# Kernel tuning notes

Measured on AMD Instinct MI355X. Metric: run time of the kernel, lower is better.

The kernel has to match this reference:

```python
import jax, jax.numpy as jnp
import numpy as np

N_HEAD = 8
DROP_RATE = 0.1


def setup_inputs() -> dict:
    key = jax.random.key(0)
    k1, k2, k3 = jax.random.split(key, 3)
    n, c, h, w = 16, 512, 32, 32
    return {
        "x": jax.random.normal(k1, (n, c, h, w), jnp.float32),
        "qkv_w": jax.random.normal(k2, (3 * c, c), jnp.float32) * 0.02,
        "qkv_b": jnp.zeros((3 * c,), jnp.float32),
        "out_w": jax.random.normal(k3, (c, c), jnp.float32) * 0.02,
        "out_b": jnp.zeros((c,), jnp.float32),
        "dropout_enabled": 0,
    }


def reference(x, qkv_w, qkv_b, out_w, out_b, dropout_enabled):
    n, c, h, w = x.shape
    hd = c // N_HEAD  # head dim
    # fused QKV 1x1 conv == per-pixel matmul: [n, 3c, h, w]
    qkv = jnp.einsum('oc,nchw->nohw', qkv_w, x) + qkv_b[None, :, None, None]
    # [n, 3*n_head, hd, h*w] -> [n, 3*n_head, h*w, hd]
    qkv = jnp.swapaxes(qkv.reshape(n, N_HEAD * 3, hd, h * w), 2, 3)
    q, k, v = jnp.split(qkv, 3, axis=1)  # each [n, n_head, hw, hd]
    scale = hd ** (-0.25)
    att = jax.nn.softmax((q * scale) @ (jnp.swapaxes(k, 2, 3) * scale), axis=3)
    y = jnp.swapaxes(att @ v, 2, 3).reshape(n, c, h, w)
    y = jnp.einsum('oc,nchw->nohw', out_w, y) + out_b[None, :, None, None]
    # Dropout2d: drops whole (n, c) channel maps
    rate = DROP_RATE * dropout_enabled
    keep = jax.random.bernoulli(jax.random.key(42), 1.0 - rate, shape=(n, c))
    y = y * keep[..., None, None] / (1.0 - rate)
    return x + y
```

## Files before the change

kernel.cpp:

```cpp
#include <hip/hip_runtime.h>

typedef short bf16x8 __attribute__((ext_vector_type(8)));
typedef float f32x4 __attribute__((ext_vector_type(4)));
typedef float f32x16 __attribute__((ext_vector_type(16)));

#define MFMA16(a,b,c) __builtin_amdgcn_mfma_f32_16x16x32_bf16((a),(b),(c),0,0,0)
#define MFMA32(a,b,c) __builtin_amdgcn_mfma_f32_32x32x16_bf16((a),(b),(c),0,0,0)

static __device__ __forceinline__ unsigned short f2bf(float f){
  unsigned u; __builtin_memcpy(&u, &f, 4);
  u += 0x7fffu + ((u >> 16) & 1u);
  return (unsigned short)(u >> 16);
}

static __device__ __forceinline__ unsigned cvtpk(float lo, float hi){
  unsigned r;
  asm volatile("v_cvt_pk_bf16_f32 %0, %1, %2" : "=v"(r) : "v"(lo), "v"(hi));
  return r;
}
static __device__ __forceinline__ void pl32swap(unsigned &a, unsigned &b){
  asm volatile("v_permlane32_swap_b32 %0, %1" : "+v"(a), "+v"(b));
}

static __device__ __forceinline__ void gload_lds16(const void* g, void* l) {
  __builtin_amdgcn_global_load_lds(
      (__attribute__((address_space(1))) void*)g,
      (__attribute__((address_space(3))) void*)l, 16, 0, 0);
}

__global__ __launch_bounds__(256) void cvt_bf16(
    const float* __restrict__ in, unsigned short* __restrict__ out, int n) {
  int i = blockIdx.x * 256 + threadIdx.x;
  if (i < n) out[i] = f2bf(in[i]);
}

__global__ __launch_bounds__(256) void transpose_cvt(
    const float* __restrict__ in, unsigned short* __restrict__ out)
{
  __shared__ unsigned short tile[32][33];
  const long base = (long)blockIdx.z * 512 * 1024;
  const int t = threadIdx.x, tx = t & 31, ty = t >> 5;
  const int c0 = blockIdx.x * 32, r0 = blockIdx.y * 32;
  const float* ib = in + base;
#pragma unroll
  for (int i = 0; i < 4; ++i)
    tile[ty + i * 8][tx] = f2bf(ib[(long)(r0 + ty + i * 8) * 1024 + c0 + tx]);
  __syncthreads();
  unsigned short* ob = out + base;
#pragma unroll
  for (int i = 0; i < 4; ++i)
    ob[(long)(c0 + ty + i * 8) * 512 + r0 + tx] = tile[tx][ty + i * 8];
}

__global__ __launch_bounds__(256, 3) void gemm_qkv(
    const unsigned short* __restrict__ A, const unsigned short* __restrict__ B,
    unsigned short* __restrict__ qkvout, const float* __restrict__ bias)
{
  const int M = 1024, K = 512;
  __shared__ unsigned short As[128 * 64];
  __shared__ unsigned short Bs[128 * 64];
  const int t = threadIdx.x, lane = t & 63, wv = t >> 6;
  const int quad = lane >> 4, ln = lane & 15;
  const int m0 = blockIdx.y * 128, n0 = blockIdx.x * 128;
  const long zb = blockIdx.z;
  A += zb * (long)M * K;

  const int srow = wv * 32 + (lane >> 3);
  const int scol = ((lane & 7) * 8) ^ ((lane >> 3) * 8);

  f32x4 zero = {0.f, 0.f, 0.f, 0.f};
  f32x4 acc[4][4];
#pragma unroll
  for (int i = 0; i < 4; ++i)
#pragma unroll
    for (int j = 0; j < 4; ++j) acc[i][j] = zero;

  const int wm = (wv & 1) * 64, wn = (wv >> 1) * 64;
  const int rsw = (ln & 7) * 8;

  for (int kt = 0; kt < K; kt += 64) {
#pragma unroll
    for (int i = 0; i < 4; ++i) {
      gload_lds16(&A[(long)(m0 + srow + i * 8) * K + kt + scol],
                  &As[(wv * 32 + i * 8) * 64]);
      gload_lds16(&B[(long)(n0 + srow + i * 8) * K + kt + scol],
                  &Bs[(wv * 32 + i * 8) * 64]);
    }
    __syncthreads();
#pragma unroll
    for (int kk = 0; kk < 64; kk += 32) {
      bf16x8 a[4], b[4];
#pragma unroll
      for (int i = 0; i < 4; ++i)
        a[i] = *(const bf16x8*)&As[(wm + i * 16 + ln) * 64 + ((kk + quad * 8) ^ rsw)];
#pragma unroll
      for (int j = 0; j < 4; ++j)
        b[j] = *(const bf16x8*)&Bs[(wn + j * 16 + ln) * 64 + ((kk + quad * 8) ^ rsw)];
#pragma unroll
      for (int i = 0; i < 4; ++i)
#pragma unroll
        for (int j = 0; j < 4; ++j)
          acc[i][j] = MFMA16(a[i], b[j], acc[i][j]);
    }
    __syncthreads();
  }

#pragma unroll
  for (int j = 0; j < 4; ++j) {
    int o = n0 + wn + j * 16 + ln;
    float bb = bias[o];
    int part = o >> 9;
    int h = (o >> 6) & 7, d = o & 63;
    float qs = (part == 0) ? 0.18033688f : 1.0f;
#pragma unroll
    for (int i = 0; i < 4; ++i) {
      int p = m0 + wm + i * 16 + quad * 4;
      f32x4 v = acc[i][j];
      if (part < 2) {
        unsigned short* dst = qkvout + (long)part * 8388608
            + ((long)(zb * 8 + h) * 1024 + p) * 64 + d;
#pragma unroll
        for (int r = 0; r < 4; ++r) dst[r * 64] = f2bf((v[r] + bb) * qs);
      } else {
        long cidx = ((long)zb * 512 + (o - 1024)) * 1024 + p;
        ushort4 st;
        st.x = f2bf(v[0] + bb); st.y = f2bf(v[1] + bb);
        st.z = f2bf(v[2] + bb); st.w = f2bf(v[3] + bb);
        *(ushort4*)&qkvout[16777216 + cidx] = st;
      }
    }
  }
}

__global__ __launch_bounds__(256, 3) void gemm_out(
    const unsigned short* __restrict__ A, const unsigned short* __restrict__ B,
    float* __restrict__ C, const float* __restrict__ bias,
    const float* __restrict__ xin, const int* __restrict__ de_ptr)
{
  const int M = 1024, K = 512;
  __shared__ unsigned short As[128 * 64];
  __shared__ unsigned short Bs[128 * 64];
  const int t = threadIdx.x, lane = t & 63, wv = t >> 6;
  const int quad = lane >> 4, ln = lane & 15;
  const int m0 = blockIdx.y * 128, n0 = blockIdx.x * 128;
  const long zb = blockIdx.z;
  A += zb * (long)M * K;
  C += zb * 512l * M;
  xin += zb * 512l * M;

  const int srow = wv * 32 + (lane >> 3);
  const int scol = ((lane & 7) * 8) ^ ((lane >> 3) * 8);

  f32x4 zero = {0.f, 0.f, 0.f, 0.f};
  f32x4 acc[4][4];
#pragma unroll
  for (int i = 0; i < 4; ++i)
#pragma unroll
    for (int j = 0; j < 4; ++j) acc[i][j] = zero;

  const int wm = (wv & 1) * 64, wn = (wv >> 1) * 64;
  const int rsw = (ln & 7) * 8;

  for (int kt = 0; kt < K; kt += 64) {
#pragma unroll
    for (int i = 0; i < 4; ++i) {
      gload_lds16(&A[(long)(m0 + srow + i * 8) * K + kt + scol],
                  &As[(wv * 32 + i * 8) * 64]);
      gload_lds16(&B[(long)(n0 + srow + i * 8) * K + kt + scol],
                  &Bs[(wv * 32 + i * 8) * 64]);
    }
    __syncthreads();
#pragma unroll
    for (int kk = 0; kk < 64; kk += 32) {
      bf16x8 a[4], b[4];
#pragma unroll
      for (int i = 0; i < 4; ++i)
        a[i] = *(const bf16x8*)&As[(wm + i * 16 + ln) * 64 + ((kk + quad * 8) ^ rsw)];
#pragma unroll
      for (int j = 0; j < 4; ++j)
        b[j] = *(const bf16x8*)&Bs[(wn + j * 16 + ln) * 64 + ((kk + quad * 8) ^ rsw)];
#pragma unroll
      for (int i = 0; i < 4; ++i)
#pragma unroll
        for (int j = 0; j < 4; ++j)
          acc[i][j] = MFMA16(a[i], b[j], acc[i][j]);
    }
    __syncthreads();
  }

  float dscale = 1.0f / (1.0f - 0.1f * (float)de_ptr[0]);

#pragma unroll
  for (int j = 0; j < 4; ++j) {
    int o = n0 + wn + j * 16 + ln;
    float bb = bias[o];
#pragma unroll
    for (int i = 0; i < 4; ++i) {
      int p = m0 + wm + i * 16 + quad * 4;
      long cidx = (long)o * M + p;
      f32x4 v = acc[i][j];
      float4 rx = *(const float4*)&xin[cidx];
      float4 st;
      st.x = rx.x + (v[0] + bb) * dscale;
      st.y = rx.y + (v[1] + bb) * dscale;
      st.z = rx.z + (v[2] + bb) * dscale;
      st.w = rx.w + (v[3] + bb) * dscale;
      *(float4*)&C[cidx] = st;
    }
  }
}

__global__ __launch_bounds__(256, 2) void attn_kernel(
    const unsigned short* __restrict__ q_pd, const unsigned short* __restrict__ k_pd,
    const unsigned short* __restrict__ v_cp, unsigned short* __restrict__ y_pc)
{
  __shared__ unsigned short Ks[2][128 * 64];
  __shared__ unsigned short Vs[2][64 * 128];
  const int t = threadIdx.x, lane = t & 63, wv = t >> 6;
  const int l31 = lane & 31, bh8 = (lane >> 5) * 8;
  const int qt = blockIdx.y >> 5;
  const int nh = blockIdx.x * 32 + (blockIdx.y & 31);
  const int n = nh >> 3, h = nh & 7;
  const int q0 = qt * 256;

  bf16x8 qa[2][4];
#pragma unroll
  for (int qg = 0; qg < 2; ++qg) {
    const unsigned short* qb =
        q_pd + ((long)nh * 1024 + q0 + wv * 64 + qg * 32 + l31) * 64;
#pragma unroll
    for (int ds = 0; ds < 4; ++ds)
      qa[qg][ds] = *(const bf16x8*)(qb + ds * 16 + bh8);
  }

  f32x16 zacc;
#pragma unroll
  for (int r = 0; r < 16; ++r) zacc[r] = 0.f;
  f32x16 o_acc[2][2];
  o_acc[0][0] = zacc; o_acc[0][1] = zacc; o_acc[1][0] = zacc; o_acc[1][1] = zacc;
  float l_acc[2] = {0.f, 0.f};

  const unsigned short* kg0 = k_pd + (long)nh * 1024 * 64;
  const unsigned short* vg0 = v_cp + ((long)n * 512 + h * 64) * 1024;

  const int krow = lane >> 3;
  const int kcol = ((lane & 7) * 8) ^ ((lane >> 3) * 8);
  const int vrow = lane >> 4;
  const int rsw = (lane & 7) * 8;

#pragma unroll
  for (int i = 0; i < 4; ++i) {
    const int vcol = ((lane & 15) * 8) ^ ((((i * 4) + vrow) & 7) * 8);
    gload_lds16(kg0 + (long)(wv * 32 + i * 8 + krow) * 64 + kcol,
                &Ks[0][(wv * 32 + i * 8) * 64]);
    gload_lds16(vg0 + (long)(wv * 16 + i * 4 + vrow) * 1024 + vcol,
                &Vs[0][(wv * 16 + i * 4) * 128]);
  }
  __syncthreads();

  union U { bf16x8 v; unsigned u[4]; };
  auto sm_pack = [&](const f32x16& sv, bf16x8* paq, float& lac) {
    float e[16];
#pragma unroll
    for (int r = 0; r < 16; ++r) e[r] = __builtin_amdgcn_exp2f(sv[r]);
    float ls = 0.f;
#pragma unroll
    for (int r = 0; r < 16; ++r) ls += e[r];
    lac += ls;
    unsigned pk4[4][2];
#pragma unroll
    for (int hh = 0; hh < 4; ++hh) {
      pk4[hh][0] = cvtpk(e[4 * hh + 0], e[4 * hh + 1]);
      pk4[hh][1] = cvtpk(e[4 * hh + 2], e[4 * hh + 3]);
    }
#pragma unroll
    for (int hk = 0; hk < 2; ++hk) {
      unsigned a0 = pk4[2 * hk + 1][0], b0 = pk4[2 * hk][0];
      unsigned a1 = pk4[2 * hk + 1][1], b1 = pk4[2 * hk][1];
      pl32swap(a0, b0); pl32swap(a1, b1);
      U u; u.u[0] = b0; u.u[1] = b1; u.u[2] = a0; u.u[3] = a1;
      paq[hk] = u.v;
    }
  };

  for (int c = 0; c < 8; ++c) {
    const int cur = c & 1;
    if (c < 7) {
      const unsigned short* kg = kg0 + (long)(c + 1) * 128 * 64;
      const unsigned short* vg = vg0 + (c + 1) * 128;
      unsigned short* KsD = Ks[cur ^ 1];
      unsigned short* VsD = Vs[cur ^ 1];
#pragma unroll
      for (int i = 0; i < 4; ++i) {
        const int vcol = ((lane & 15) * 8) ^ ((((i * 4) + vrow) & 7) * 8);
        gload_lds16(kg + (long)(wv * 32 + i * 8 + krow) * 64 + kcol,
                    &KsD[(wv * 32 + i * 8) * 64]);
        gload_lds16(vg + (long)(wv * 16 + i * 4 + vrow) * 1024 + vcol,
                    &VsD[(wv * 16 + i * 4) * 128]);
      }
    }
    const unsigned short* KsC = Ks[cur];
    const unsigned short* VsC = Vs[cur];

#pragma unroll
    for (int kgi = 0; kgi < 4; ++kgi) {
      f32x16 s0 = zacc, s1 = zacc;
#pragma unroll
      for (int ds = 0; ds < 4; ++ds) {
        bf16x8 ka = *(const bf16x8*)&KsC[(kgi * 32 + l31) * 64 + ((ds * 16 + bh8) ^ rsw)];
        s0 = MFMA32(ka, qa[0][ds], s0);
        s1 = MFMA32(ka, qa[1][ds], s1);
      }
      bf16x8 pa[2][2];
      sm_pack(s0, pa[0], l_acc[0]);
      sm_pack(s1, pa[1], l_acc[1]);
#pragma unroll
      for (int dg = 0; dg < 2; ++dg)
#pragma unroll
        for (int hk = 0; hk < 2; ++hk) {
          bf16x8 va = *(const bf16x8*)
              &VsC[(dg * 32 + l31) * 128 + (((kgi * 2 + hk) * 16 + bh8) ^ rsw)];
          o_acc[dg][0] = MFMA32(va, pa[0][hk], o_acc[dg][0]);
          o_acc[dg][1] = MFMA32(va, pa[1][hk], o_acc[dg][1]);
        }
    }
    __syncthreads();
  }

#pragma unroll
  for (int qg = 0; qg < 2; ++qg) {
    float la = l_acc[qg];
    la += __shfl_xor(la, 32);
    float linv = 1.0f / la;
    const int q = q0 + wv * 64 + qg * 32 + l31;
    unsigned short* yb = y_pc + ((long)n * 1024 + q) * 512 + h * 64;
#pragma unroll
    for (int dg = 0; dg < 2; ++dg) {
      f32x16 o = o_acc[dg][qg];
#pragma unroll
      for (int rq = 0; rq < 4; ++rq) {
        int d0 = dg * 32 + rq * 8 + (bh8 >> 1);
        ushort4 st;
        st.x = f2bf(o[rq * 4 + 0] * linv);
        st.y = f2bf(o[rq * 4 + 1] * linv);
        st.z = f2bf(o[rq * 4 + 2] * linv);
        st.w = f2bf(o[rq * 4 + 3] * linv);
        *(ushort4*)&yb[d0] = st;
      }
    }
  }
}

extern "C" void kernel_launch(void* const* d_in, const int* in_sizes, int n_in,
                              void* d_out, int out_size, void* d_ws, size_t ws_size,
                              hipStream_t stream) {
  (void)in_sizes; (void)n_in; (void)out_size; (void)ws_size;
  const float* x     = (const float*)d_in[0];
  const float* qkv_w = (const float*)d_in[1];
  const float* qkv_b = (const float*)d_in[2];
  const float* out_w = (const float*)d_in[3];
  const float* out_b = (const float*)d_in[4];
  const int* de = (const int*)d_in[5];
  float* out = (float*)d_out;
  unsigned short* ws = (unsigned short*)d_ws;

  unsigned short* xT   = ws;
  unsigned short* qkv  = ws + 8388608;
  unsigned short* y_pc = ws;
  unsigned short* wq   = ws + 33554432;
  unsigned short* wo   = wq + 786432;

  cvt_bf16<<<3072, 256, 0, stream>>>(qkv_w, wq, 786432);
  cvt_bf16<<<1024, 256, 0, stream>>>(out_w, wo, 262144);

  transpose_cvt<<<dim3(32, 16, 16), 256, 0, stream>>>(x, xT);

  gemm_qkv<<<dim3(12, 8, 16), 256, 0, stream>>>(xT, wq, qkv, qkv_b);

  attn_kernel<<<dim3(4, 128), 256, 0, stream>>>(
      qkv, qkv + 8388608, qkv + 16777216, y_pc);

  gemm_out<<<dim3(4, 8, 16), 256, 0, stream>>>(
      y_pc, wo, out, out_b, x, de);
}
```

Before: 206.9 us.

## Remap GEMM block order, widen V LDS swizzle, add MFMA priority hints

Both GEMM kernels remap the linear block index so consecutive dispatched blocks are spread in an XCD-aware pattern (stride of 8 groups), aiming for better L2 locality of shared A/B tiles per XCD. The attention kernel widens the V-tile LDS XOR swizzle from 8 to 16 column groups to reduce bank conflicts on V reads. It also wraps MFMA sections with s_setprio to favor matrix issue across waves. The remap assumes specific grid dimensions and an 8-way XCD split.

```diff
diff --git a/kernel.cpp b/kernel.cpp
--- a/kernel.cpp
+++ b/kernel.cpp
@@ -61,8 +61,11 @@
   __shared__ unsigned short Bs[128 * 64];
   const int t = threadIdx.x, lane = t & 63, wv = t >> 6;
   const int quad = lane >> 4, ln = lane & 15;
-  const int m0 = blockIdx.y * 128, n0 = blockIdx.x * 128;
-  const long zb = blockIdx.z;
+
+  const int L = blockIdx.x + 12 * blockIdx.y + 96 * blockIdx.z;
+  const int v = (L & 7) * 192 + (L >> 3);
+  const int m0 = ((v / 12) & 7) * 128, n0 = (v % 12) * 128;
+  const long zb = v / 96;
   A += zb * (long)M * K;
 
   const int srow = wv * 32 + (lane >> 3);
@@ -115,17 +118,17 @@
 #pragma unroll
     for (int i = 0; i < 4; ++i) {
       int p = m0 + wm + i * 16 + quad * 4;
-      f32x4 v = acc[i][j];
+      f32x4 vv = acc[i][j];
       if (part < 2) {
         unsigned short* dst = qkvout + (long)part * 8388608
             + ((long)(zb * 8 + h) * 1024 + p) * 64 + d;
 #pragma unroll
-        for (int r = 0; r < 4; ++r) dst[r * 64] = f2bf((v[r] + bb) * qs);
+        for (int r = 0; r < 4; ++r) dst[r * 64] = f2bf((vv[r] + bb) * qs);
       } else {
         long cidx = ((long)zb * 512 + (o - 1024)) * 1024 + p;
         ushort4 st;
-        st.x = f2bf(v[0] + bb); st.y = f2bf(v[1] + bb);
-        st.z = f2bf(v[2] + bb); st.w = f2bf(v[3] + bb);
+        st.x = f2bf(vv[0] + bb); st.y = f2bf(vv[1] + bb);
+        st.z = f2bf(vv[2] + bb); st.w = f2bf(vv[3] + bb);
         *(ushort4*)&qkvout[16777216 + cidx] = st;
       }
     }
@@ -142,8 +145,11 @@
   __shared__ unsigned short Bs[128 * 64];
   const int t = threadIdx.x, lane = t & 63, wv = t >> 6;
   const int quad = lane >> 4, ln = lane & 15;
-  const int m0 = blockIdx.y * 128, n0 = blockIdx.x * 128;
-  const long zb = blockIdx.z;
+
+  const int L = blockIdx.x + 4 * blockIdx.y + 32 * blockIdx.z;
+  const int v = (L & 7) * 64 + (L >> 3);
+  const int m0 = ((v >> 2) & 7) * 128, n0 = (v & 3) * 128;
+  const long zb = v >> 5;
   A += zb * (long)M * K;
   C += zb * 512l * M;
   xin += zb * 512l * M;
@@ -198,13 +204,13 @@
     for (int i = 0; i < 4; ++i) {
       int p = m0 + wm + i * 16 + quad * 4;
       long cidx = (long)o * M + p;
-      f32x4 v = acc[i][j];
+      f32x4 vv = acc[i][j];
       float4 rx = *(const float4*)&xin[cidx];
       float4 st;
-      st.x = rx.x + (v[0] + bb) * dscale;
-      st.y = rx.y + (v[1] + bb) * dscale;
-      st.z = rx.z + (v[2] + bb) * dscale;
-      st.w = rx.w + (v[3] + bb) * dscale;
+      st.x = rx.x + (vv[0] + bb) * dscale;
+      st.y = rx.y + (vv[1] + bb) * dscale;
+      st.z = rx.z + (vv[2] + bb) * dscale;
+      st.w = rx.w + (vv[3] + bb) * dscale;
       *(float4*)&C[cidx] = st;
     }
   }
@@ -247,13 +253,15 @@
   const int kcol = ((lane & 7) * 8) ^ ((lane >> 3) * 8);
   const int vrow = lane >> 4;
   const int rsw = (lane & 7) * 8;
+  const int vrsw = (l31 & 15) * 8;
 
 #pragma unroll
   for (int i = 0; i < 4; ++i) {
-    const int vcol = ((lane & 15) * 8) ^ ((((i * 4) + vrow) & 7) * 8);
+    const int vr = i * 4 + vrow;
+    const int vcol = ((lane & 15) ^ vr) * 8;
     gload_lds16(kg0 + (long)(wv * 32 + i * 8 + krow) * 64 + kcol,
                 &Ks[0][(wv * 32 + i * 8) * 64]);
-    gload_lds16(vg0 + (long)(wv * 16 + i * 4 + vrow) * 1024 + vcol,
+    gload_lds16(vg0 + (long)(wv * 16 + vr) * 1024 + vcol,
                 &Vs[0][(wv * 16 + i * 4) * 128]);
   }
   __syncthreads();
@@ -292,10 +300,11 @@
       unsigned short* VsD = Vs[cur ^ 1];
 #pragma unroll
       for (int i = 0; i < 4; ++i) {
-        const int vcol = ((lane & 15) * 8) ^ ((((i * 4) + vrow) & 7) * 8);
+        const int vr = i * 4 + vrow;
+        const int vcol = ((lane & 15) ^ vr) * 8;
         gload_lds16(kg + (long)(wv * 32 + i * 8 + krow) * 64 + kcol,
                     &KsD[(wv * 32 + i * 8) * 64]);
-        gload_lds16(vg + (long)(wv * 16 + i * 4 + vrow) * 1024 + vcol,
+        gload_lds16(vg + (long)(wv * 16 + vr) * 1024 + vcol,
                     &VsD[(wv * 16 + i * 4) * 128]);
       }
     }
@@ -305,24 +314,28 @@
 #pragma unroll
     for (int kgi = 0; kgi < 4; ++kgi) {
       f32x16 s0 = zacc, s1 = zacc;
+      __builtin_amdgcn_s_setprio(1);
 #pragma unroll
       for (int ds = 0; ds < 4; ++ds) {
         bf16x8 ka = *(const bf16x8*)&KsC[(kgi * 32 + l31) * 64 + ((ds * 16 + bh8) ^ rsw)];
         s0 = MFMA32(ka, qa[0][ds], s0);
         s1 = MFMA32(ka, qa[1][ds], s1);
       }
+      __builtin_amdgcn_s_setprio(0);
       bf16x8 pa[2][2];
       sm_pack(s0, pa[0], l_acc[0]);
       sm_pack(s1, pa[1], l_acc[1]);
+      __builtin_amdgcn_s_setprio(1);
 #pragma unroll
       for (int dg = 0; dg < 2; ++dg)
 #pragma unroll
         for (int hk = 0; hk < 2; ++hk) {
           bf16x8 va = *(const bf16x8*)
-              &VsC[(dg * 32 + l31) * 128 + (((kgi * 2 + hk) * 16 + bh8) ^ rsw)];
+              &VsC[(dg * 32 + l31) * 128 + (((kgi * 2 + hk) * 16 + bh8) ^ vrsw)];
           o_acc[dg][0] = MFMA32(va, pa[0][hk], o_acc[dg][0]);
           o_acc[dg][1] = MFMA32(va, pa[1][hk], o_acc[dg][1]);
         }
+      __builtin_amdgcn_s_setprio(0);
     }
     __syncthreads();
   }
```

After: 191.3 us. -7.6%, faster.
